# Kernel optimization log

Hardware: AMD Instinct MI355X
Metric: run time of the kernel (lower is better)

The kernel has to match this reference:

```python
import jax, jax.numpy as jnp
import numpy as np

G = 64      # norm_groups
T = 5       # Newton-Schulz iterations
EPS = 1e-5


def setup_inputs() -> dict:
    key = jax.random.key(0)
    weight = jax.random.normal(key, (2048, 18432), dtype=jnp.float32)
    return {"weight": weight}


def reference(weight):
    out_ch = weight.shape[0]
    # Z: [G, c, d] with c = out_ch // G, d = prod(rest)
    Z = weight.reshape(G, out_ch // G, -1)
    Zc = Z - jnp.mean(Z, axis=-1, keepdims=True)
    # S = Zc @ Zc^T : [G, c, c]
    S = jnp.einsum('gcd,ged->gce', Zc, Zc)
    c = S.shape[-1]
    eye = jnp.eye(c, dtype=S.dtype)
    S = S + EPS * eye
    # Frobenius norm per group, keepdim -> [G,1,1]
    norm_S = jnp.sqrt(jnp.sum(S * S, axis=(1, 2), keepdims=True))
    S = S / norm_S
    # Newton-Schulz: B_{t+1} = 1.5*B_t - 0.5 * B_t^3 @ S
    B = jnp.broadcast_to(eye, S.shape)
    for _ in range(T):
        B3 = jnp.matmul(jnp.matmul(B, B), B)
        B = 1.5 * B - 0.5 * jnp.matmul(B3, S)
    W = jnp.matmul(B, Zc) / jnp.sqrt(norm_S)
    return W.reshape(weight.shape)
```

## Files before the change

### kernel.cpp

```cpp
#include <hip/hip_runtime.h>

#define G 64
#define C 32
#define D 18432
#define KSUB 128
#define PSTR 136
#define PLANE (32 * PSTR)
#define EPS 1e-5f
#define NS_ITERS 5

typedef __attribute__((ext_vector_type(8))) short short8v;
typedef __attribute__((ext_vector_type(4))) float float4v;

__device__ __forceinline__ void split3(float x, unsigned short& h1,
                                       unsigned short& h2, unsigned short& h3) {
    unsigned int u = __float_as_uint(x);
    unsigned int m1 = u & 0xffff0000u;
    float r1 = x - __uint_as_float(m1);
    unsigned int u2 = __float_as_uint(r1);
    unsigned int m2 = u2 & 0xffff0000u;
    float r2 = r1 - __uint_as_float(m2);
    h1 = (unsigned short)(m1 >> 16);
    h2 = (unsigned short)(m2 >> 16);
    h3 = (unsigned short)(__float_as_uint(r2) >> 16);
}

template <int NCHT>
__global__ __launch_bounds__(256) void k1_gram(const float* __restrict__ W,
                                               float* __restrict__ psum,
                                               float* __restrict__ prow) {
    constexpr int TD  = D / NCHT;
    constexpr int NST = TD / KSUB;

    __shared__ __align__(16) unsigned short lds_u[3 * PLANE];

    const int ch   = blockIdx.x;
    const int g    = blockIdx.y;
    const int bid  = g * NCHT + ch;
    const int tid  = threadIdx.x;
    const int lane = tid & 63;
    const int wave = tid >> 6;
    const float* Zg = W + (size_t)g * C * D + (size_t)ch * TD;

    const int r  = tid >> 3;
    const int cb = (tid & 7) * 16;
    const float* srcRow = Zg + (size_t)r * D;

    const int lh = lane & 15;
    const int kb = (lane >> 4) * 8;
    const int kbase = wave * 32;

    float4v acc[2][2];
#pragma unroll
    for (int a = 0; a < 2; ++a)
#pragma unroll
        for (int b = 0; b < 2; ++b) acc[a][b] = (float4v)0.f;
    float rs = 0.f;

    float4 cur[4], nxt[4];
#pragma unroll
    for (int i = 0; i < 4; ++i)
        cur[i] = *(const float4*)(srcRow + cb + 4 * i);

#pragma unroll
    for (int st = 0; st < NST; ++st) {
        if (st + 1 < NST) {
            const float* s = srcRow + (st + 1) * KSUB + cb;
#pragma unroll
            for (int i = 0; i < 4; ++i) nxt[i] = *(const float4*)(s + 4 * i);
        }
        float x[16];
#pragma unroll
        for (int i = 0; i < 4; ++i) {
            x[4 * i + 0] = cur[i].x; x[4 * i + 1] = cur[i].y;
            x[4 * i + 2] = cur[i].z; x[4 * i + 3] = cur[i].w;
        }
        unsigned short h1[16], h2[16], h3[16];
#pragma unroll
        for (int i = 0; i < 16; ++i) {
            rs += x[i];
            split3(x[i], h1[i], h2[i], h3[i]);
        }
        if (st) __syncthreads();
        const int widx = r * PSTR + cb;
#pragma unroll
        for (int q = 0; q < 2; ++q) {
            short8v v1, v2, v3;
#pragma unroll
            for (int j = 0; j < 8; ++j) {
                v1[j] = (short)h1[8 * q + j];
                v2[j] = (short)h2[8 * q + j];
                v3[j] = (short)h3[8 * q + j];
            }
            *(short8v*)&lds_u[widx + 8 * q]             = v1;
            *(short8v*)&lds_u[PLANE + widx + 8 * q]     = v2;
            *(short8v*)&lds_u[2 * PLANE + widx + 8 * q] = v3;
        }
        __syncthreads();
        short8v fr[2][3];
#pragma unroll
        for (int h = 0; h < 2; ++h)
#pragma unroll
            for (int p = 0; p < 3; ++p)
                fr[h][p] = *(const short8v*)&lds_u[p * PLANE + (16 * h + lh) * PSTR + kbase + kb];
#pragma unroll
        for (int a = 0; a < 2; ++a)
#pragma unroll
            for (int b = 0; b < 2; ++b) {
                float4v t = acc[a][b];
                t = __builtin_amdgcn_mfma_f32_16x16x32_bf16(fr[a][0], fr[b][0], t, 0, 0, 0);
                t = __builtin_amdgcn_mfma_f32_16x16x32_bf16(fr[a][0], fr[b][1], t, 0, 0, 0);
                t = __builtin_amdgcn_mfma_f32_16x16x32_bf16(fr[a][1], fr[b][0], t, 0, 0, 0);
                t = __builtin_amdgcn_mfma_f32_16x16x32_bf16(fr[a][1], fr[b][1], t, 0, 0, 0);
                t = __builtin_amdgcn_mfma_f32_16x16x32_bf16(fr[a][0], fr[b][2], t, 0, 0, 0);
                t = __builtin_amdgcn_mfma_f32_16x16x32_bf16(fr[a][2], fr[b][0], t, 0, 0, 0);
                acc[a][b] = t;
            }
#pragma unroll
        for (int i = 0; i < 4; ++i) cur[i] = nxt[i];
    }

#pragma unroll
    for (int off = 1; off <= 4; off <<= 1) rs += __shfl_xor(rs, off, 64);
    if ((tid & 7) == 0) prow[(size_t)bid * C + r] = rs;

    __syncthreads();
    float* red = (float*)lds_u;
#pragma unroll
    for (int a = 0; a < 2; ++a)
#pragma unroll
        for (int b = 0; b < 2; ++b)
#pragma unroll
            for (int j = 0; j < 4; ++j) {
                int row = 16 * a + ((lane >> 4) << 2) + j;
                int col = 16 * b + lh;
                red[wave * 1056 + row * 33 + col] = acc[a][b][j];
            }
    __syncthreads();
#pragma unroll
    for (int k = 0; k < 4; ++k) {
        int el = tid + 256 * k;
        int row = el >> 5, col = el & 31;
        int o = row * 33 + col;
        float sv = red[o] + red[1056 + o] + red[2112 + o] + red[3168 + o];
        psum[(size_t)bid * (C * C) + el] = sv;
    }
}

template <int NCHT>
__global__ __launch_bounds__(256) void k2_ns(const float* __restrict__ psum,
                                             const float* __restrict__ prow,
                                             float* __restrict__ MT,
                                             float* __restrict__ vout) {
    __shared__ float S[C][C + 1];
    __shared__ float B[C][C + 1];
    __shared__ float T1[C][C + 1];
    __shared__ float T2[C][C + 1];
    __shared__ float mean[C];
    __shared__ float redw[4];
    __shared__ float normsh;

    const int g   = blockIdx.x;
    const int tid = threadIdx.x;
    const int e   = tid & 31;
    const int cbq = tid >> 5;

    float selt[4];
#pragma unroll
    for (int k = 0; k < 4; ++k) {
        int el = tid + 256 * k;
        float s = 0.f;
#pragma unroll
        for (int ch = 0; ch < NCHT; ++ch)
            s += psum[((size_t)g * NCHT + ch) * (C * C) + el];
        selt[k] = s;
    }
    if (tid < C) {
        float s = 0.f;
#pragma unroll
        for (int ch = 0; ch < NCHT; ++ch)
            s += prow[((size_t)g * NCHT + ch) * C + tid];
        mean[tid] = s / (float)D;
    }
    __syncthreads();

    float ss = 0.f;
#pragma unroll
    for (int k = 0; k < 4; ++k) {
        int el = tid + 256 * k;
        int c = el >> 5;
        float sv = selt[k] - (float)D * mean[c] * mean[e];
        if (c == e) sv += EPS;
        S[c][e] = sv;
        ss = fmaf(sv, sv, ss);
    }
#pragma unroll
    for (int off = 32; off >= 1; off >>= 1) ss += __shfl_xor(ss, off, 64);
    if ((tid & 63) == 0) redw[tid >> 6] = ss;
    __syncthreads();
    if (tid == 0) normsh = sqrtf(redw[0] + redw[1] + redw[2] + redw[3]);
    __syncthreads();
    const float inv_norm = 1.0f / normsh;
#pragma unroll
    for (int k = 0; k < 4; ++k) {
        int c = cbq + 8 * k;
        S[c][e] *= inv_norm;
        B[c][e] = (c == e) ? 1.f : 0.f;
    }
    __syncthreads();

    for (int it = 0; it < NS_ITERS; ++it) {
#pragma unroll
        for (int k = 0; k < 4; ++k) {
            int c = cbq + 8 * k;
            float s = 0.f;
            for (int kk = 0; kk < C; ++kk)
                s = fmaf(B[c][kk], B[kk][e], s);
            T1[c][e] = s;
        }
        __syncthreads();
#pragma unroll
        for (int k = 0; k < 4; ++k) {
            int c = cbq + 8 * k;
            float s = 0.f;
            for (int kk = 0; kk < C; ++kk)
                s = fmaf(T1[c][kk], B[kk][e], s);
            T2[c][e] = s;
        }
        __syncthreads();
        float pv[4];
#pragma unroll
        for (int k = 0; k < 4; ++k) {
            int c = cbq + 8 * k;
            float s = 0.f;
            for (int kk = 0; kk < C; ++kk)
                s = fmaf(T2[c][kk], S[kk][e], s);
            pv[k] = s;
        }
#pragma unroll
        for (int k = 0; k < 4; ++k) {
            int c = cbq + 8 * k;
            B[c][e] = 1.5f * B[c][e] - 0.5f * pv[k];
        }
        __syncthreads();
    }

    const float invs = 1.0f / sqrtf(normsh);
#pragma unroll
    for (int k = 0; k < 4; ++k) {
        int c = cbq + 8 * k;
        MT[(size_t)g * (C * C) + e * C + c] = B[c][e] * invs;
    }
    if (tid < C) {
        float s = 0.f;
        for (int ee = 0; ee < C; ++ee)
            s = fmaf(B[tid][ee] * invs, mean[ee], s);
        vout[(size_t)g * C + tid] = s;
    }
}

__global__ __launch_bounds__(256) void k3_apply(const float* __restrict__ W,
                                                const float* __restrict__ MT,
                                                const float* __restrict__ vv,
                                                float* __restrict__ out) {
    const int g  = blockIdx.y;
    const int d0 = blockIdx.x * 512 + (int)threadIdx.x * 2;
    const float* Zg = W + (size_t)g * C * D + d0;
    const float* Mg = MT + (size_t)g * (C * C);

    float accx[C], accy[C];
#pragma unroll
    for (int r = 0; r < C; ++r) { accx[r] = 0.f; accy[r] = 0.f; }

    for (int e = 0; e < C; ++e) {
        float2 z = *(const float2*)(Zg + (size_t)e * D);
#pragma unroll
        for (int r = 0; r < C; ++r) {
            float m = Mg[e * C + r];
            accx[r] = fmaf(m, z.x, accx[r]);
            accy[r] = fmaf(m, z.y, accy[r]);
        }
    }

    float* Og = out + (size_t)g * C * D + d0;
#pragma unroll
    for (int r = 0; r < C; ++r) {
        float vr = vv[g * C + r];
        float2 o = make_float2(accx[r] - vr, accy[r] - vr);
        double dv;
        __builtin_memcpy(&dv, &o, 8);
        __builtin_nontemporal_store(dv, (double*)(Og + (size_t)r * D));
    }
}

extern "C" void kernel_launch(void* const* d_in, const int* in_sizes, int n_in,
                              void* d_out, int out_size, void* d_ws, size_t ws_size,
                              hipStream_t stream) {
    const float* w = (const float*)d_in[0];
    float* out = (float*)d_out;

    const size_t need36 = ((size_t)G * 36 * (C * C + C) + (size_t)G * (C * C + C)) * sizeof(float);
    const bool use36 = (ws_size >= need36);
    const int nch = use36 ? 36 : 16;

    float* psum = (float*)d_ws;
    float* prow = psum + (size_t)(G * nch) * (C * C);
    float* MT   = prow + (size_t)(G * nch) * C;
    float* vv   = MT   + (size_t)G * (C * C);

    if (use36) {
        k1_gram<36><<<dim3(36, G), 256, 0, stream>>>(w, psum, prow);
        k2_ns<36>  <<<G,           256, 0, stream>>>(psum, prow, MT, vv);
    } else {
        k1_gram<16><<<dim3(16, G), 256, 0, stream>>>(w, psum, prow);
        k2_ns<16>  <<<G,           256, 0, stream>>>(psum, prow, MT, vv);
    }
    k3_apply<<<dim3(D / 512, G), 256, 0, stream>>>(w, MT, vv, out);
}
```

Baseline: 104.8 us.

## Loosen LDS barriers in gram kernel, use plain stores, and use 24 chunks

In the gram kernel, the full __syncthreads pair is replaced with raw s_barrier calls. The write-side barrier waits on lgkmcnt and the pre-write barrier has no wait, so split-word packing can overlap outstanding loads. The apply kernel's output stores change from nontemporal to ordinary float2 stores. The split-K chunk count drops from 36 to 24, giving fewer, longer blocks and fewer partial sums for the NS kernel to reduce. The pre-write barrier no longer waits on outstanding LDS reads, which could be a correctness risk.

```diff
diff --git a/kernel.cpp b/kernel.cpp
--- a/kernel.cpp
+++ b/kernel.cpp
@@ -75,28 +75,31 @@
             x[4 * i + 0] = cur[i].x; x[4 * i + 1] = cur[i].y;
             x[4 * i + 2] = cur[i].z; x[4 * i + 3] = cur[i].w;
         }
-        unsigned short h1[16], h2[16], h3[16];
-#pragma unroll
-        for (int i = 0; i < 16; ++i) {
-            rs += x[i];
-            split3(x[i], h1[i], h2[i], h3[i]);
-        }
-        if (st) __syncthreads();
+        short8v s1[2], s2[2], s3[2];
+#pragma unroll
+        for (int q = 0; q < 2; ++q) {
+#pragma unroll
+            for (int j = 0; j < 8; ++j) {
+                unsigned short h1, h2, h3;
+                float xv = x[8 * q + j];
+                rs += xv;
+                split3(xv, h1, h2, h3);
+                s1[q][j] = (short)h1; s2[q][j] = (short)h2; s3[q][j] = (short)h3;
+            }
+        }
+        asm volatile("" ::: "memory");
+        __builtin_amdgcn_s_barrier();
+        asm volatile("" ::: "memory");
         const int widx = r * PSTR + cb;
 #pragma unroll
         for (int q = 0; q < 2; ++q) {
-            short8v v1, v2, v3;
-#pragma unroll
-            for (int j = 0; j < 8; ++j) {
-                v1[j] = (short)h1[8 * q + j];
-                v2[j] = (short)h2[8 * q + j];
-                v3[j] = (short)h3[8 * q + j];
-            }
-            *(short8v*)&lds_u[widx + 8 * q]             = v1;
-            *(short8v*)&lds_u[PLANE + widx + 8 * q]     = v2;
-            *(short8v*)&lds_u[2 * PLANE + widx + 8 * q] = v3;
-        }
-        __syncthreads();
+            *(short8v*)&lds_u[widx + 8 * q]             = s1[q];
+            *(short8v*)&lds_u[PLANE + widx + 8 * q]     = s2[q];
+            *(short8v*)&lds_u[2 * PLANE + widx + 8 * q] = s3[q];
+        }
+        asm volatile("s_waitcnt lgkmcnt(0)" ::: "memory");
+        __builtin_amdgcn_s_barrier();
+        asm volatile("" ::: "memory");
         short8v fr[2][3];
 #pragma unroll
         for (int h = 0; h < 2; ++h)
@@ -287,9 +290,7 @@
     for (int r = 0; r < C; ++r) {
         float vr = vv[g * C + r];
         float2 o = make_float2(accx[r] - vr, accy[r] - vr);
-        double dv;
-        __builtin_memcpy(&dv, &o, 8);
-        __builtin_nontemporal_store(dv, (double*)(Og + (size_t)r * D));
+        *(float2*)(Og + (size_t)r * D) = o;
     }
 }
 
@@ -299,18 +300,18 @@
     const float* w = (const float*)d_in[0];
     float* out = (float*)d_out;
 
-    const size_t need36 = ((size_t)G * 36 * (C * C + C) + (size_t)G * (C * C + C)) * sizeof(float);
-    const bool use36 = (ws_size >= need36);
-    const int nch = use36 ? 36 : 16;
+    const size_t need24 = ((size_t)G * 24 * (C * C + C) + (size_t)G * (C * C + C)) * sizeof(float);
+    const bool use24 = (ws_size >= need24);
+    const int nch = use24 ? 24 : 16;
 
     float* psum = (float*)d_ws;
     float* prow = psum + (size_t)(G * nch) * (C * C);
     float* MT   = prow + (size_t)(G * nch) * C;
     float* vv   = MT   + (size_t)G * (C * C);
 
-    if (use36) {
-        k1_gram<36><<<dim3(36, G), 256, 0, stream>>>(w, psum, prow);
-        k2_ns<36>  <<<G,           256, 0, stream>>>(psum, prow, MT, vv);
+    if (use24) {
+        k1_gram<24><<<dim3(24, G), 256, 0, stream>>>(w, psum, prow);
+        k2_ns<24>  <<<G,           256, 0, stream>>>(psum, prow, MT, vv);
     } else {
         k1_gram<16><<<dim3(16, G), 256, 0, stream>>>(w, psum, prow);
         k2_ns<16>  <<<G,           256, 0, stream>>>(psum, prow, MT, vv);
```

Result: no change. 103.4 us (-1.3%).
